# Kernel optimization log

Measured on AMD Instinct MI355X. Metric: run time of the kernel, lower is better.

## Reference

```python
import jax, jax.numpy as jnp
import numpy as np

N_TYPES = 4  # global / and / or / leaf node types (indep_weights)


def gcn_layer(x, W_stack, b, edge_src, edge_dst, edge_w, labels, num_nodes):
    # Per-node-type dense projection: compute all 4 projections, then select by label.
    # all4: [4, N, out]
    all4 = jnp.einsum('nd,kdo->kno', x, W_stack)
    support = jnp.take_along_axis(all4, labels[None, :, None].astype(jnp.int32), axis=0)[0]  # [N, out]
    # Sparse adjacency propagation: out[dst] += w * support[src]  (torch.spmm equivalent)
    msgs = support[edge_src] * edge_w[:, None]  # [E, out]
    agg = jax.ops.segment_sum(msgs, edge_dst, num_segments=num_nodes)
    return agg + b


def setup_inputs() -> dict:
    key = jax.random.key(0)
    ks = jax.random.split(key, 12)
    N, E = 50000, 1600000
    nfeat, nhid, nclass = 256, 256, 64
    x = jax.random.normal(ks[0], (N, nfeat), dtype=jnp.float32)
    edge_src = jax.random.randint(ks[1], (E,), 0, N, dtype=jnp.int32)
    edge_dst = jax.random.randint(ks[2], (E,), 0, N, dtype=jnp.int32)
    edge_w = jax.random.uniform(ks[3], (E,), dtype=jnp.float32)
    labels = jax.random.randint(ks[4], (N,), 0, N_TYPES, dtype=jnp.int32)
    def winit(k, fi, fo):
        s = 1.0 / np.sqrt(fo)
        return jax.random.uniform(k, (N_TYPES, fi, fo), minval=-s, maxval=s, dtype=jnp.float32)
    def binit(k, fo):
        s = 1.0 / np.sqrt(fo)
        return jax.random.uniform(k, (fo,), minval=-s, maxval=s, dtype=jnp.float32)
    return {
        'x': x, 'edge_src': edge_src, 'edge_dst': edge_dst, 'edge_w': edge_w, 'labels': labels,
        'W1': winit(ks[5], nfeat, nhid), 'b1': binit(ks[6], nhid),
        'W2': winit(ks[7], nhid, nhid), 'b2': binit(ks[8], nhid),
        'W3': winit(ks[9], nhid, nclass), 'b3': binit(ks[10], nclass),
    }


def reference(x, edge_src, edge_dst, edge_w, labels, W1, b1, W2, b2, W3, b3):
    N = x.shape[0]
    h = jax.nn.relu(gcn_layer(x, W1, b1, edge_src, edge_dst, edge_w, labels, N))
    # F.dropout with p=0 (module default) is identity
    h = jax.nn.relu(gcn_layer(h, W2, b2, edge_src, edge_dst, edge_w, labels, N))
    out = gcn_layer(h, W3, b3, edge_src, edge_dst, edge_w, labels, N)
    return out
```

## Files before the change

### kernel.cpp

```cpp
#include <hip/hip_runtime.h>
#include <hip/hip_bf16.h>

#define NT 4
#define FEAT 256
#define OUT3 64

typedef __bf16 bf16x8 __attribute__((ext_vector_type(8)));
typedef float  f32x4  __attribute__((ext_vector_type(4)));

__device__ inline unsigned int f2bf_bits(float f) {
    __hip_bfloat16 h = __float2bfloat16(f);
    unsigned short u;
    __builtin_memcpy(&u, &h, 2);
    return (unsigned int)u;
}
__device__ inline float bfl(unsigned int u) { return __uint_as_float(u << 16); }
__device__ inline float bfh(unsigned int u) { return __uint_as_float(u & 0xffff0000u); }
__device__ __host__ inline int nat_of(int p) {
    int lo = p & 63;
    return (p & ~63) | (((lo & 3) << 4) | (lo >> 2));
}

__global__ __launch_bounds__(512) void pass_a(const int* __restrict__ dst,
                                              const int* __restrict__ labels,
                                              int* __restrict__ bcnt, int* __restrict__ lc,
                                              int E, int N) {
    __shared__ int h[256];
    __shared__ int lh[NT];
    int tid = threadIdx.x;
    if (tid < 256) h[tid] = 0;
    if (tid < NT) lh[tid] = 0;
    __syncthreads();
    int base = blockIdx.x * 4096;
#pragma unroll
    for (int k = 0; k < 8; ++k) {
        int e = base + k * 512 + tid;
        if (e < E) atomicAdd(&h[((unsigned)dst[e]) >> 8], 1);
    }
#pragma unroll
    for (int k = 0; k < 8; ++k) {
        int i = base + k * 512 + tid;
        if (i < N) atomicAdd(&lh[labels[i]], 1);
    }
    __syncthreads();
    if (tid < 256) { int v = h[tid]; if (v) atomicAdd(&bcnt[tid], v); }
    if (tid < NT) { int v = lh[tid]; if (v) atomicAdd(&lc[tid], v); }
}

__global__ __launch_bounds__(256) void scan_master(
    const int* __restrict__ bcnt, const int* __restrict__ lc,
    int* __restrict__ boff, int* __restrict__ gcur, int* __restrict__ rowoff,
    int* __restrict__ lstart, int NB, int N, int E) {
    __shared__ int s[256];
    int tid = threadIdx.x;
    int own = (tid < NB) ? bcnt[tid] : 0;
    s[tid] = own;
    __syncthreads();
    for (int d = 1; d < 256; d <<= 1) {
        int v = (tid >= d) ? s[tid - d] : 0;
        __syncthreads();
        s[tid] += v;
        __syncthreads();
    }
    int excl = s[tid] - own;
    if (tid < NB) { boff[tid] = excl; gcur[tid] = excl; }
    if (tid == 0) {
        boff[NB] = E; rowoff[N] = E;
        int run = 0;
        for (int l = 0; l < NT; ++l) {
            lstart[l] = run;
            run += (lc[l] + 63) & ~63;
        }
    }
}

__global__ void scatter_nodes(const int* __restrict__ labels, const int* __restrict__ lstart,
                              int* __restrict__ lcur, int* __restrict__ iperm, int N) {
    int n = blockIdx.x * 256 + threadIdx.x;
    int lab = (n < N) ? labels[n] : -1;
    int lane = threadIdx.x & 63;
    for (int l = 0; l < NT; ++l) {
        unsigned long long m = __ballot(lab == l);
        if (m == 0ull) continue;
        int leader = __builtin_ctzll(m);
        int base = 0;
        if (lane == leader) base = atomicAdd(&lcur[l], (int)__popcll(m));
        base = __shfl(base, leader, 64);
        if (lab == l) {
            int prefix = (int)__popcll(m & ((1ull << lane) - 1ull));
            iperm[n] = lstart[l] + base + prefix;
        }
    }
}

__global__ __launch_bounds__(512) void fuse_a(
    const int* __restrict__ src, const int* __restrict__ dst, const float* __restrict__ w,
    const int* __restrict__ iperm, int* __restrict__ gcur, uint2* __restrict__ earr, int E,
    const float* __restrict__ x, unsigned short* __restrict__ actLo,
    unsigned short* __restrict__ actHi, int total4,
    const float* __restrict__ W1, const float* __restrict__ W2, const float* __restrict__ W3,
    const float* __restrict__ b1, const float* __restrict__ b2,
    unsigned short* __restrict__ W1b, unsigned short* __restrict__ W2b,
    unsigned short* __restrict__ W3b, float* __restrict__ biasPerm,
    int nbEB, int nbX) {
    int tid = threadIdx.x;
    int blk = (int)blockIdx.x;
    if (blk < nbEB) {
        __shared__ int h[256];
        __shared__ int basearr[256];
        if (tid < 256) h[tid] = 0;
        __syncthreads();
        int base = blk * 4096;
        int b[8], rank[8], px[8]; float wv[8];
#pragma unroll
        for (int k = 0; k < 8; ++k) {
            int e = base + k * 512 + tid;
            if (e < E) {
                int d = dst[e];
                b[k] = ((unsigned)d) >> 8;
                px[k] = iperm[src[e]] | ((d & 255) << 16);
                wv[k] = w[e];
                rank[k] = atomicAdd(&h[b[k]], 1);
            } else b[k] = -1;
        }
        __syncthreads();
        if (tid < 256) { int c = h[tid]; basearr[tid] = c ? atomicAdd(&gcur[tid], c) : 0; }
        __syncthreads();
#pragma unroll
        for (int k = 0; k < 8; ++k) {
            if (b[k] >= 0) {
                int pos = basearr[b[k]] + rank[k];
                earr[pos] = make_uint2((unsigned)px[k], __float_as_uint(wv[k]));
            }
        }
    } else if (blk < nbEB + nbX) {
        int i = (blk - nbEB) * 512 + tid;
        if (i < total4) {
            float4 v = ((const float4*)x)[i];
            unsigned int lo = f2bf_bits(v.x) | (f2bf_bits(v.y) << 16);
            unsigned int hi = f2bf_bits(v.z) | (f2bf_bits(v.w) << 16);
            int slot = iperm[i >> 6];
            unsigned short* dp = ((i & 63) >= 32) ? actHi : actLo;
            ((uint2*)dp)[(size_t)slot * 32 + (i & 31)] = make_uint2(lo, hi);
        }
    } else {
        const int S = NT * FEAT * FEAT;
        const int S3 = NT * FEAT * OUT3;
        int idx = (blk - nbEB - nbX) * 512 + tid;
        if (idx < 2 * S + S3) {
            const float* W; unsigned short* D; int OUTF; int t; bool remap;
            if (idx < S)          { W = W1; D = W1b; OUTF = FEAT; t = idx;         remap = false; }
            else if (idx < 2 * S) { W = W2; D = W2b; OUTF = FEAT; t = idx - S;     remap = true; }
            else                  { W = W3; D = W3b; OUTF = OUT3; t = idx - 2 * S; remap = true; }
            int n = t % OUTF;
            int r = t / OUTF;
            int j = r & 7, q = (r >> 3) & 3, k0 = (r >> 5) & 7, lab = r >> 8;
            int k_slot = k0 * 32 + q * 8 + j;
            int k_src = remap ? nat_of(k_slot) : k_slot;
            float f = W[((size_t)(lab * FEAT + k_src)) * OUTF + n];
            D[(((size_t)lab * 8 + k0) * OUTF + n) * 32 + q * 8 + j] = (unsigned short)f2bf_bits(f);
        } else {
            int p2 = idx - (2 * S + S3);
            if (p2 < 256) biasPerm[p2] = b1[nat_of(p2)];
            else if (p2 < 512) biasPerm[p2] = b2[nat_of(p2 - 256)];
        }
    }
}

__device__ void bucket_sort_body(int b, const uint2* __restrict__ earr,
                                 const int* __restrict__ boff, int* __restrict__ rowoff,
                                 unsigned int* __restrict__ edata, int N) {
    int s = boff[b], e = boff[b + 1];
    __shared__ int cnt[256], off[256];
    int tid = threadIdx.x;
    cnt[tid] = 0;
    __syncthreads();
    for (int i = s + tid; i < e; i += 256) atomicAdd(&cnt[(earr[i].x >> 16) & 255], 1);
    __syncthreads();
    off[tid] = cnt[tid];
    __syncthreads();
    for (int d = 1; d < 256; d <<= 1) {
        int v = (tid >= d) ? off[tid - d] : 0;
        __syncthreads();
        off[tid] += v;
        __syncthreads();
    }
    int excl = off[tid] - cnt[tid];
    int node = b * 256 + tid;
    if (node < N) rowoff[node] = s + excl;
    off[tid] = excl;
    __syncthreads();
    for (int i = s + tid; i < e; i += 256) {
        uint2 r = earr[i];
        int d = (r.x >> 16) & 255;
        int k = atomicAdd(&off[d], 1);
        edata[s + k] = (f2bf_bits(__uint_as_float(r.y)) << 16) | (r.x & 0xffff);
    }
}

__device__ void proj256_body(int gb,
                             const unsigned short* __restrict__ actLo,
                             const unsigned short* __restrict__ actHi,
                             const unsigned short* __restrict__ Wswz,
                             const int* __restrict__ lstart,
                             unsigned short* __restrict__ supLo,
                             unsigned short* __restrict__ supHi) {
    int warp = threadIdx.x >> 6;
    int lane = threadIdx.x & 63;
    int m0 = gb * 64;
    int lab = (m0 >= lstart[1]) + (m0 >= lstart[2]) + (m0 >= lstart[3]);
    int q = lane >> 4, c = lane & 15;
    int n0 = warp * 64;

    const unsigned short* aLo = actLo + (size_t)(m0 + c) * 128 + q * 8;
    const unsigned short* aHi = actHi + (size_t)(m0 + c) * 128 + q * 8;
    const unsigned short* bb = Wswz + (size_t)lab * FEAT * 256 + (size_t)(n0 + c) * 32 + q * 8;

    f32x4 acc[4][4] = {};
#pragma unroll
    for (int k0 = 0; k0 < 8; ++k0) {
        const unsigned short* abase = (k0 < 4) ? aLo : aHi;
        int koff = (k0 & 3) * 32;
        bf16x8 a[4];
#pragma unroll
        for (int t = 0; t < 4; ++t) a[t] = *(const bf16x8*)(abase + (size_t)t * 2048 + koff);
        const unsigned short* bk = bb + (size_t)k0 * 32 * 256;
#pragma unroll
        for (int u = 0; u < 4; ++u) {
            bf16x8 bfrag = *(const bf16x8*)(bk + u * 512);
#pragma unroll
            for (int t = 0; t < 4; ++t)
                acc[t][u] = __builtin_amdgcn_mfma_f32_16x16x32_bf16(a[t], bfrag, acc[t][u], 0, 0, 0);
        }
    }
    uint2* ov = (uint2*)((n0 >= 128) ? supHi : supLo);
    int cix = ((n0 & 64) >> 2) + c;
#pragma unroll
    for (int t = 0; t < 4; ++t) {
#pragma unroll
        for (int r = 0; r < 4; ++r) {
            int row = m0 + t * 16 + q * 4 + r;
            unsigned int lo = f2bf_bits(acc[t][0][r]) | (f2bf_bits(acc[t][1][r]) << 16);
            unsigned int hi = f2bf_bits(acc[t][2][r]) | (f2bf_bits(acc[t][3][r]) << 16);
            ov[(size_t)row * 32 + cix] = make_uint2(lo, hi);
        }
    }
}

__global__ __launch_bounds__(256) void fuse_b(
    const uint2* __restrict__ earr, const int* __restrict__ boff,
    int* __restrict__ rowoff, unsigned int* __restrict__ edata, int N, int NB,
    const unsigned short* __restrict__ actLo, const unsigned short* __restrict__ actHi,
    const unsigned short* __restrict__ Wswz, const int* __restrict__ lstart,
    unsigned short* __restrict__ supLo, unsigned short* __restrict__ supHi) {
    int blk = (int)blockIdx.x;
    if (blk < NB) bucket_sort_body(blk, earr, boff, rowoff, edata, N);
    else proj256_body(blk - NB, actLo, actHi, Wswz, lstart, supLo, supHi);
}

__global__ __launch_bounds__(256) void proj256_kernel(
    const unsigned short* __restrict__ actLo, const unsigned short* __restrict__ actHi,
    const unsigned short* __restrict__ Wswz, const int* __restrict__ lstart,
    unsigned short* __restrict__ supLo, unsigned short* __restrict__ supHi) {
    proj256_body((int)blockIdx.x, actLo, actHi, Wswz, lstart, supLo, supHi);
}

__global__ __launch_bounds__(256) void proj64_kernel(
    const unsigned short* __restrict__ actLo, const unsigned short* __restrict__ actHi,
    const unsigned short* __restrict__ Wswz, const int* __restrict__ lstart,
    unsigned short* __restrict__ outp) {
    int warp = threadIdx.x >> 6;
    int lane = threadIdx.x & 63;
    int m0 = blockIdx.x * 64;
    int lab = (m0 >= lstart[1]) + (m0 >= lstart[2]) + (m0 >= lstart[3]);
    int q = lane >> 4, c = lane & 15;
    int mb = m0 + warp * 16;

    const unsigned short* aLo = actLo + (size_t)(mb + c) * 128 + q * 8;
    const unsigned short* aHi = actHi + (size_t)(mb + c) * 128 + q * 8;
    const unsigned short* bb = Wswz + (size_t)lab * FEAT * OUT3 + (size_t)c * 32 + q * 8;

    f32x4 acc[4] = {};
#pragma unroll
    for (int k0 = 0; k0 < 8; ++k0) {
        const unsigned short* abase = (k0 < 4) ? aLo : aHi;
        bf16x8 a = *(const bf16x8*)(abase + (k0 & 3) * 32);
        const unsigned short* bk = bb + (size_t)k0 * 32 * OUT3;
#pragma unroll
        for (int u = 0; u < 4; ++u) {
            bf16x8 bfrag = *(const bf16x8*)(bk + u * 512);
            acc[u] = __builtin_amdgcn_mfma_f32_16x16x32_bf16(a, bfrag, acc[u], 0, 0, 0);
        }
    }
    uint2* ov = (uint2*)outp;
#pragma unroll
    for (int r = 0; r < 4; ++r) {
        int row = mb + q * 4 + r;
        unsigned int lo = f2bf_bits(acc[0][r]) | (f2bf_bits(acc[1][r]) << 16);
        unsigned int hi = f2bf_bits(acc[2][r]) | (f2bf_bits(acc[3][r]) << 16);
        ov[(size_t)row * 16 + c] = make_uint2(lo, hi);
    }
}

__global__ __launch_bounds__(256) void agg256h_kernel(
    const unsigned int* __restrict__ sup, const int* __restrict__ rowoff,
    const unsigned int* __restrict__ edata, const int* __restrict__ iperm,
    const float* __restrict__ biasHalf, unsigned int* __restrict__ outp, int N) {
    int warp = __builtin_amdgcn_readfirstlane((int)(threadIdx.x >> 6));
    int node = (int)blockIdx.x * 4 + warp;
    if (node >= N) return;
    int lane = threadIdx.x & 63;
    int s = __builtin_amdgcn_readfirstlane(rowoff[node]);
    int e = __builtin_amdgcn_readfirstlane(rowoff[node + 1]);
    int slot = __builtin_amdgcn_readfirstlane(iperm[node]);
    float a0 = 0.f, a1 = 0.f;
    int j = s;
    for (; j + 16 <= e; j += 16) {
        unsigned int ed[16], v[16];
#pragma unroll
        for (int u = 0; u < 16; ++u) ed[u] = edata[j + u];
#pragma unroll
        for (int u = 0; u < 16; ++u) v[u] = sup[(size_t)(ed[u] & 0xffff) * 64 + lane];
#pragma unroll
        for (int u = 0; u < 16; ++u) {
            float w = __uint_as_float(ed[u] & 0xffff0000u);
            a0 += w * bfl(v[u]); a1 += w * bfh(v[u]);
        }
    }
    if (j < e) {
        unsigned int ed[16], v[16]; float wm[16];
#pragma unroll
        for (int u = 0; u < 16; ++u) {
            int jj = j + u;
            int jc = (jj < e) ? jj : e - 1;
            ed[u] = edata[jc];
            wm[u] = (jj < e) ? __uint_as_float(ed[u] & 0xffff0000u) : 0.f;
        }
#pragma unroll
        for (int u = 0; u < 16; ++u) v[u] = sup[(size_t)(ed[u] & 0xffff) * 64 + lane];
#pragma unroll
        for (int u = 0; u < 16; ++u) { a0 += wm[u] * bfl(v[u]); a1 += wm[u] * bfh(v[u]); }
    }
    float2 b = ((const float2*)biasHalf)[lane];
    a0 = fmaxf(a0 + b.x, 0.f);
    a1 = fmaxf(a1 + b.y, 0.f);
    outp[(size_t)slot * 64 + lane] = f2bf_bits(a0) | (f2bf_bits(a1) << 16);
}

__global__ __launch_bounds__(256) void agg64_kernel(
    const unsigned short* __restrict__ sup, const int* __restrict__ rowoff,
    const unsigned int* __restrict__ edata, const float* __restrict__ b3,
    float* __restrict__ outp, int N) {
    int warp = __builtin_amdgcn_readfirstlane((int)(threadIdx.x >> 6));
    int node = (int)blockIdx.x * 4 + warp;
    if (node >= N) return;
    int lane = threadIdx.x & 63;
    int s = __builtin_amdgcn_readfirstlane(rowoff[node]);
    int e = __builtin_amdgcn_readfirstlane(rowoff[node + 1]);
    float a = 0.f;
    int j = s;
    for (; j + 8 <= e; j += 8) {
        unsigned int ed[8]; unsigned short v[8];
#pragma unroll
        for (int u = 0; u < 8; ++u) ed[u] = edata[j + u];
#pragma unroll
        for (int u = 0; u < 8; ++u) v[u] = sup[(size_t)(ed[u] & 0xffff) * 64 + lane];
#pragma unroll
        for (int u = 0; u < 8; ++u)
            a += __uint_as_float(ed[u] & 0xffff0000u) * __uint_as_float((unsigned int)v[u] << 16);
    }
    if (j < e) {
        unsigned int ed[8]; float wm[8]; unsigned short v[8];
#pragma unroll
        for (int u = 0; u < 8; ++u) {
            int jj = j + u;
            int jc = (jj < e) ? jj : e - 1;
            ed[u] = edata[jc];
            wm[u] = (jj < e) ? __uint_as_float(ed[u] & 0xffff0000u) : 0.f;
        }
#pragma unroll
        for (int u = 0; u < 8; ++u) v[u] = sup[(size_t)(ed[u] & 0xffff) * 64 + lane];
#pragma unroll
        for (int u = 0; u < 8; ++u)
            a += wm[u] * __uint_as_float((unsigned int)v[u] << 16);
    }
    int natp = (((lane & 3) << 4) | (lane >> 2));
    outp[(size_t)node * 64 + natp] = a + b3[natp];
}

extern "C" void kernel_launch(void* const* d_in, const int* in_sizes, int n_in,
                              void* d_out, int out_size, void* d_ws, size_t ws_size,
                              hipStream_t stream) {
    const float* x        = (const float*)d_in[0];
    const int*   edge_src = (const int*)d_in[1];
    const int*   edge_dst = (const int*)d_in[2];
    const float* edge_w   = (const float*)d_in[3];
    const int*   labels   = (const int*)d_in[4];
    const float* W1 = (const float*)d_in[5];
    const float* b1 = (const float*)d_in[6];
    const float* W2 = (const float*)d_in[7];
    const float* b2 = (const float*)d_in[8];
    const float* W3 = (const float*)d_in[9];
    const float* b3 = (const float*)d_in[10];

    const int N = in_sizes[0] / FEAT;
    const int E = in_sizes[1];
    const int NB = (N + 255) >> 8;
    const int G64 = (N + NT * 64 + 63) / 64;
    const int slotCap = G64 * 64;

    char* p = (char*)d_ws;
    auto alloc = [&](size_t bytes) -> char* {
        char* r = p;
        p += (bytes + 255) & ~(size_t)255;
        return r;
    };
    unsigned short* bufA = (unsigned short*)alloc((size_t)slotCap * FEAT * 2);
    unsigned short* bufB = (unsigned short*)alloc((size_t)slotCap * FEAT * 2);
    unsigned short* W1b  = (unsigned short*)alloc((size_t)NT * FEAT * FEAT * 2);
    unsigned short* W2b  = (unsigned short*)alloc((size_t)NT * FEAT * FEAT * 2);
    unsigned short* W3b  = (unsigned short*)alloc((size_t)NT * FEAT * OUT3 * 2);
    float*        biasPerm = (float*)alloc(512 * 4);
    int*          rowoff = (int*)alloc((size_t)(N + 1) * 4);
    unsigned int* edata  = (unsigned int*)alloc((size_t)E * 4);
    int*          iperm  = (int*)alloc((size_t)N * 4);
    int*          counters = (int*)alloc(264 * 4);
    int*          boff   = (int*)alloc(257 * 4);
    int*          gcur   = (int*)alloc(256 * 4);
    int*          lstart = (int*)alloc(64);
    int* bcnt = counters;
    int* lc   = counters + 256;
    int* lcur = counters + 260;

    unsigned short* actLo = bufA;
    unsigned short* actHi = bufA + (size_t)slotCap * 128;
    unsigned short* supLo = bufB;
    unsigned short* supHi = bufB + (size_t)slotCap * 128;
    uint2* earr = (uint2*)d_out;

    const int nbEB = (E + 4095) / 4096;
    const int total4 = N * 64;
    const int nbX = (total4 + 511) / 512;
    const int totW = 2 * NT * FEAT * FEAT + NT * FEAT * OUT3 + 512;
    const int nbW = (totW + 511) / 512;

    hipMemsetAsync(counters, 0, 264 * 4, stream);
    pass_a<<<nbEB, 512, 0, stream>>>(edge_dst, labels, bcnt, lc, E, N);
    scan_master<<<1, 256, 0, stream>>>(bcnt, lc, boff, gcur, rowoff, lstart, NB, N, E);
    scatter_nodes<<<(N + 255) / 256, 256, 0, stream>>>(labels, lstart, lcur, iperm, N);
    fuse_a<<<nbEB + nbX + nbW, 512, 0, stream>>>(
        edge_src, edge_dst, edge_w, iperm, gcur, earr, E,
        x, actLo, actHi, total4,
        W1, W2, W3, b1, b2, W1b, W2b, W3b, biasPerm, nbEB, nbX);

    const int aggGrid = (N + 3) / 4;
    fuse_b<<<NB + G64, 256, 0, stream>>>(earr, boff, rowoff, edata, N, NB,
                                         actLo, actHi, W1b, lstart, supLo, supHi);
    agg256h_kernel<<<aggGrid, 256, 0, stream>>>((const unsigned int*)supLo, rowoff, edata, iperm,
                                                biasPerm + 0, (unsigned int*)actLo, N);
    agg256h_kernel<<<aggGrid, 256, 0, stream>>>((const unsigned int*)supHi, rowoff, edata, iperm,
                                                biasPerm + 128, (unsigned int*)actHi, N);
    proj256_kernel<<<G64, 256, 0, stream>>>(actLo, actHi, W2b, lstart, supLo, supHi);
    agg256h_kernel<<<aggGrid, 256, 0, stream>>>((const unsigned int*)supLo, rowoff, edata, iperm,
                                                biasPerm + 256, (unsigned int*)actLo, N);
    agg256h_kernel<<<aggGrid, 256, 0, stream>>>((const unsigned int*)supHi, rowoff, edata, iperm,
                                                biasPerm + 384, (unsigned int*)actHi, N);
    proj64_kernel<<<G64, 256, 0, stream>>>(actLo, actHi, W3b, lstart, bufB);
    agg64_kernel<<<aggGrid, 256, 0, stream>>>(bufB, rowoff, edata, b3, (float*)d_out, N);
}
```

Before: 482.3 us.

## Use fixed-capacity dst buckets to drop histogram pass; add nontemporal loads/stores

```diff
diff --git a/kernel.cpp b/kernel.cpp
--- a/kernel.cpp
+++ b/kernel.cpp
@@ -4,9 +4,11 @@
 #define NT 4
 #define FEAT 256
 #define OUT3 64
+#define CAP 10240
 
 typedef __bf16 bf16x8 __attribute__((ext_vector_type(8)));
 typedef float  f32x4  __attribute__((ext_vector_type(4)));
+typedef unsigned long long u64;
 
 __device__ inline unsigned int f2bf_bits(float f) {
     __hip_bfloat16 h = __float2bfloat16(f);
@@ -20,62 +22,38 @@
     int lo = p & 63;
     return (p & ~63) | (((lo & 3) << 4) | (lo >> 2));
 }
-
-__global__ __launch_bounds__(512) void pass_a(const int* __restrict__ dst,
-                                              const int* __restrict__ labels,
-                                              int* __restrict__ bcnt, int* __restrict__ lc,
-                                              int E, int N) {
-    __shared__ int h[256];
+__device__ inline u64 ntl64(const void* p) { return __builtin_nontemporal_load((const u64*)p); }
+__device__ inline int ntl32i(const void* p) { return __builtin_nontemporal_load((const int*)p); }
+__device__ inline float ntlf(const void* p) { return __builtin_nontemporal_load((const float*)p); }
+__device__ inline void nts64(void* p, u64 v) { __builtin_nontemporal_store(v, (u64*)p); }
+__device__ inline void nts32(void* p, unsigned int v) { __builtin_nontemporal_store(v, (unsigned int*)p); }
+__device__ inline void ntsf(void* p, float v) { __builtin_nontemporal_store(v, (float*)p); }
+__device__ inline void nts16(void* p, unsigned short v) { __builtin_nontemporal_store(v, (unsigned short*)p); }
+
+__global__ __launch_bounds__(512) void label_hist(const int* __restrict__ labels,
+                                                  int* __restrict__ lc, int N) {
     __shared__ int lh[NT];
     int tid = threadIdx.x;
-    if (tid < 256) h[tid] = 0;
     if (tid < NT) lh[tid] = 0;
     __syncthreads();
     int base = blockIdx.x * 4096;
-#pragma unroll
-    for (int k = 0; k < 8; ++k) {
-        int e = base + k * 512 + tid;
-        if (e < E) atomicAdd(&h[((unsigned)dst[e]) >> 8], 1);
-    }
 #pragma unroll
     for (int k = 0; k < 8; ++k) {
         int i = base + k * 512 + tid;
         if (i < N) atomicAdd(&lh[labels[i]], 1);
     }
     __syncthreads();
-    if (tid < 256) { int v = h[tid]; if (v) atomicAdd(&bcnt[tid], v); }
     if (tid < NT) { int v = lh[tid]; if (v) atomicAdd(&lc[tid], v); }
 }
 
-__global__ __launch_bounds__(256) void scan_master(
-    const int* __restrict__ bcnt, const int* __restrict__ lc,
-    int* __restrict__ boff, int* __restrict__ gcur, int* __restrict__ rowoff,
-    int* __restrict__ lstart, int NB, int N, int E) {
-    __shared__ int s[256];
-    int tid = threadIdx.x;
-    int own = (tid < NB) ? bcnt[tid] : 0;
-    s[tid] = own;
-    __syncthreads();
-    for (int d = 1; d < 256; d <<= 1) {
-        int v = (tid >= d) ? s[tid - d] : 0;
-        __syncthreads();
-        s[tid] += v;
-        __syncthreads();
-    }
-    int excl = s[tid] - own;
-    if (tid < NB) { boff[tid] = excl; gcur[tid] = excl; }
-    if (tid == 0) {
-        boff[NB] = E; rowoff[N] = E;
+__global__ void scatter_nodes(const int* __restrict__ labels, const int* __restrict__ lc,
+                              int* __restrict__ lcur, int* __restrict__ iperm, int N) {
+    int lst[NT];
+    {
         int run = 0;
-        for (int l = 0; l < NT; ++l) {
-            lstart[l] = run;
-            run += (lc[l] + 63) & ~63;
-        }
-    }
-}
-
-__global__ void scatter_nodes(const int* __restrict__ labels, const int* __restrict__ lstart,
-                              int* __restrict__ lcur, int* __restrict__ iperm, int N) {
+#pragma unroll
+        for (int l = 0; l < NT; ++l) { lst[l] = run; run += (lc[l] + 63) & ~63; }
+    }
     int n = blockIdx.x * 256 + threadIdx.x;
     int lab = (n < N) ? labels[n] : -1;
     int lane = threadIdx.x & 63;
@@ -88,14 +66,14 @@
         base = __shfl(base, leader, 64);
         if (lab == l) {
             int prefix = (int)__popcll(m & ((1ull << lane) - 1ull));
-            iperm[n] = lstart[l] + base + prefix;
+            iperm[n] = lst[l] + base + prefix;
         }
     }
 }
 
 __global__ __launch_bounds__(512) void fuse_a(
     const int* __restrict__ src, const int* __restrict__ dst, const float* __restrict__ w,
-    const int* __restrict__ iperm, int* __restrict__ gcur, uint2* __restrict__ earr, int E,
+    const int* __restrict__ iperm, int* __restrict__ gcur, u64* __restrict__ earr, int E,
     const float* __restrict__ x, unsigned short* __restrict__ actLo,
     unsigned short* __restrict__ actHi, int total4,
     const float* __restrict__ W1, const float* __restrict__ W2, const float* __restrict__ W3,
@@ -116,10 +94,10 @@
         for (int k = 0; k < 8; ++k) {
             int e = base + k * 512 + tid;
             if (e < E) {
-                int d = dst[e];
+                int d = ntl32i(dst + e);
                 b[k] = ((unsigned)d) >> 8;
-                px[k] = iperm[src[e]] | ((d & 255) << 16);
-                wv[k] = w[e];
+                px[k] = iperm[ntl32i(src + e)] | ((d & 255) << 16);
+                wv[k] = ntlf(w + e);
                 rank[k] = atomicAdd(&h[b[k]], 1);
             } else b[k] = -1;
         }
@@ -129,19 +107,22 @@
 #pragma unroll
         for (int k = 0; k < 8; ++k) {
             if (b[k] >= 0) {
-                int pos = basearr[b[k]] + rank[k];
-                earr[pos] = make_uint2((unsigned)px[k], __float_as_uint(wv[k]));
+                size_t pos = (size_t)b[k] * CAP + basearr[b[k]] + rank[k];
+                nts64(&earr[pos], (u64)(unsigned)px[k] | ((u64)__float_as_uint(wv[k]) << 32));
             }
         }
     } else if (blk < nbEB + nbX) {
         int i = (blk - nbEB) * 512 + tid;
         if (i < total4) {
-            float4 v = ((const float4*)x)[i];
-            unsigned int lo = f2bf_bits(v.x) | (f2bf_bits(v.y) << 16);
-            unsigned int hi = f2bf_bits(v.z) | (f2bf_bits(v.w) << 16);
+            const u64* xp = (const u64*)x + (size_t)i * 2;
+            u64 w0 = ntl64(xp), w1 = ntl64(xp + 1);
+            float f0 = __uint_as_float((unsigned)w0), f1 = __uint_as_float((unsigned)(w0 >> 32));
+            float f2 = __uint_as_float((unsigned)w1), f3 = __uint_as_float((unsigned)(w1 >> 32));
+            unsigned int lo = f2bf_bits(f0) | (f2bf_bits(f1) << 16);
+            unsigned int hi = f2bf_bits(f2) | (f2bf_bits(f3) << 16);
             int slot = iperm[i >> 6];
-            unsigned short* dp = ((i & 63) >= 32) ? actHi : actLo;
-            ((uint2*)dp)[(size_t)slot * 32 + (i & 31)] = make_uint2(lo, hi);
+            u64* dp = (u64*)(((i & 63) >= 32) ? actHi : actLo);
+            nts64(dp + (size_t)slot * 32 + (i & 31), (u64)lo | ((u64)hi << 32));
         }
     } else {
         const int S = NT * FEAT * FEAT;
@@ -157,8 +138,9 @@
             int j = r & 7, q = (r >> 3) & 3, k0 = (r >> 5) & 7, lab = r >> 8;
             int k_slot = k0 * 32 + q * 8 + j;
             int k_src = remap ? nat_of(k_slot) : k_slot;
-            float f = W[((size_t)(lab * FEAT + k_src)) * OUTF + n];
-            D[(((size_t)lab * 8 + k0) * OUTF + n) * 32 + q * 8 + j] = (unsigned short)f2bf_bits(f);
+            float f = ntlf(&W[((size_t)(lab * FEAT + k_src)) * OUTF + n]);
+            nts16(&D[(((size_t)lab * 8 + k0) * OUTF + n) * 32 + q * 8 + j],
+                  (unsigned short)f2bf_bits(f));
         } else {
             int p2 = idx - (2 * S + S3);
             if (p2 < 256) biasPerm[p2] = b1[nat_of(p2)];
@@ -167,17 +149,23 @@
     }
 }
 
-__device__ void bucket_sort_body(int b, const uint2* __restrict__ earr,
-                                 const int* __restrict__ boff, int* __restrict__ rowoff,
+__device__ void bucket_sort_body(int b, const u64* __restrict__ earr,
+                                 const int* __restrict__ gcur,
+                                 int* __restrict__ rs, int* __restrict__ re,
                                  unsigned int* __restrict__ edata, int N) {
-    int s = boff[b], e = boff[b + 1];
-    __shared__ int cnt[256], off[256];
+    int s = b * CAP;
+    int cnt = gcur[b];
+    int e = s + cnt;
+    __shared__ int cntS[256], off[256];
     int tid = threadIdx.x;
-    cnt[tid] = 0;
-    __syncthreads();
-    for (int i = s + tid; i < e; i += 256) atomicAdd(&cnt[(earr[i].x >> 16) & 255], 1);
-    __syncthreads();
-    off[tid] = cnt[tid];
+    cntS[tid] = 0;
+    __syncthreads();
+    for (int i = s + tid; i < e; i += 256) {
+        u64 r = ntl64(&earr[i]);
+        atomicAdd(&cntS[((unsigned)r >> 16) & 255], 1);
+    }
+    __syncthreads();
+    off[tid] = cntS[tid];
     __syncthreads();
     for (int d = 1; d < 256; d <<= 1) {
         int v = (tid >= d) ? off[tid - d] : 0;
@@ -185,16 +173,18 @@
         off[tid] += v;
         __syncthreads();
     }
-    int excl = off[tid] - cnt[tid];
+    int excl = off[tid] - cntS[tid];
     int node = b * 256 + tid;
-    if (node < N) rowoff[node] = s + excl;
+    if (node < N) { rs[node] = s + excl; re[node] = s + excl + cntS[tid]; }
     off[tid] = excl;
     __syncthreads();
     for (int i = s + tid; i < e; i += 256) {
-        uint2 r = earr[i];
-        int d = (r.x >> 16) & 255;
-        int k = atomicAdd(&off[d], 1);
-        edata[s + k] = (f2bf_bits(__uint_as_float(r.y)) << 16) | (r.x & 0xffff);
+        u64 r = ntl64(&earr[i]);
+        unsigned int lo32 = (unsigned int)r;
+        int d2 = (lo32 >> 16) & 255;
+        int k = atomicAdd(&off[d2], 1);
+        nts32(&edata[s + k],
+              (f2bf_bits(__uint_as_float((unsigned)(r >> 32))) << 16) | (lo32 & 0xffff));
     }
 }
 
@@ -202,13 +192,14 @@
                              const unsigned short* __restrict__ actLo,
                              const unsigned short* __restrict__ actHi,
                              const unsigned short* __restrict__ Wswz,
-                             const int* __restrict__ lstart,
+                             const int* __restrict__ lc,
                              unsigned short* __restrict__ supLo,
                              unsigned short* __restrict__ supHi) {
     int warp = threadIdx.x >> 6;
     int lane = threadIdx.x & 63;
     int m0 = gb * 64;
-    int lab = (m0 >= lstart[1]) + (m0 >= lstart[2]) + (m0 >= lstart[3]);
+    int c0 = (lc[0] + 63) & ~63, c1 = (lc[1] + 63) & ~63, c2 = (lc[2] + 63) & ~63;
+    int lab = (m0 >= c0) + (m0 >= c0 + c1) + (m0 >= c0 + c1 + c2);
     int q = lane >> 4, c = lane & 15;
     int n0 = warp * 64;
 
@@ -233,7 +224,7 @@
                 acc[t][u] = __builtin_amdgcn_mfma_f32_16x16x32_bf16(a[t], bfrag, acc[t][u], 0, 0, 0);
         }
     }
-    uint2* ov = (uint2*)((n0 >= 128) ? supHi : supLo);
+    u64* ov = (u64*)((n0 >= 128) ? supHi : supLo);
     int cix = ((n0 & 64) >> 2) + c;
 #pragma unroll
     for (int t = 0; t < 4; ++t) {
@@ -242,37 +233,39 @@
             int row = m0 + t * 16 + q * 4 + r;
             unsigned int lo = f2bf_bits(acc[t][0][r]) | (f2bf_bits(acc[t][1][r]) << 16);
             unsigned int hi = f2bf_bits(acc[t][2][r]) | (f2bf_bits(acc[t][3][r]) << 16);
-            ov[(size_t)row * 32 + cix] = make_uint2(lo, hi);
+            nts64(&ov[(size_t)row * 32 + cix], (u64)lo | ((u64)hi << 32));
         }
     }
 }
 
 __global__ __launch_bounds__(256) void fuse_b(
-    const uint2* __restrict__ earr, const int* __restrict__ boff,
-    int* __restrict__ rowoff, unsigned int* __restrict__ edata, int N, int NB,
+    const u64* __restrict__ earr, const int* __restrict__ gcur,
+    int* __restrict__ rs, int* __restrict__ re, unsigned int* __restrict__ edata,
+    int N, int NB,
     const unsigned short* __restrict__ actLo, const unsigned short* __restrict__ actHi,
-    const unsigned short* __restrict__ Wswz, const int* __restrict__ lstart,
+    const unsigned short* __restrict__ Wswz, const int* __restrict__ lc,
     unsigned short* __restrict__ supLo, unsigned short* __restrict__ supHi) {
     int blk = (int)blockIdx.x;
-    if (blk < NB) bucket_sort_body(blk, earr, boff, rowoff, edata, N);
-    else proj256_body(blk - NB, actLo, actHi, Wswz, lstart, supLo, supHi);
+    if (blk < NB) bucket_sort_body(blk, earr, gcur, rs, re, edata, N);
+    else proj256_body(blk - NB, actLo, actHi, Wswz, lc, supLo, supHi);
 }
 
 __global__ __launch_bounds__(256) void proj256_kernel(
     const unsigned short* __restrict__ actLo, const unsigned short* __restrict__ actHi,
-    const unsigned short* __restrict__ Wswz, const int* __restrict__ lstart,
+    const unsigned short* __restrict__ Wswz, const int* __restrict__ lc,
     unsigned short* __restrict__ supLo, unsigned short* __restrict__ supHi) {
-    proj256_body((int)blockIdx.x, actLo, actHi, Wswz, lstart, supLo, supHi);
+    proj256_body((int)blockIdx.x, actLo, actHi, Wswz, lc, supLo, supHi);
 }
 
 __global__ __launch_bounds__(256) void proj64_kernel(
     const unsigned short* __restrict__ actLo, const unsigned short* __restrict__ actHi,
-    const unsigned short* __restrict__ Wswz, const int* __restrict__ lstart,
+    const unsigned short* __restrict__ Wswz, const int* __restrict__ lc,
     unsigned short* __restrict__ outp) {
     int warp = threadIdx.x >> 6;
     int lane = threadIdx.x & 63;
     int m0 = blockIdx.x * 64;
-    int lab = (m0 >= lstart[1]) + (m0 >= lstart[2]) + (m0 >= lstart[3]);
+    int c0 = (lc[0] + 63) & ~63, c1 = (lc[1] + 63) & ~63, c2 = (lc[2] + 63) & ~63;
+    int lab = (m0 >= c0) + (m0 >= c0 + c1) + (m0 >= c0 + c1 + c2);
     int q = lane >> 4, c = lane & 15;
     int mb = m0 + warp * 16;
 
@@ -292,26 +285,27 @@
             acc[u] = __builtin_amdgcn_mfma_f32_16x16x32_bf16(a, bfrag, acc[u], 0, 0, 0);
         }
     }
-    uint2* ov = (uint2*)outp;
+    u64* ov = (u64*)outp;
 #pragma unroll
     for (int r = 0; r < 4; ++r) {
         int row = mb + q * 4 + r;
         unsigned int lo = f2bf_bits(acc[0][r]) | (f2bf_bits(acc[1][r]) << 16);
         unsigned int hi = f2bf_bits(acc[2][r]) | (f2bf_bits(acc[3][r]) << 16);
-        ov[(size_t)row * 16 + c] = make_uint2(lo, hi);
+        nts64(&ov[(size_t)row * 16 + c], (u64)lo | ((u64)hi << 32));
     }
 }
 
 __global__ __launch_bounds__(256) void agg256h_kernel(
-    const unsigned int* __restrict__ sup, const int* __restrict__ rowoff,
-    const unsigned int* __restrict__ edata, const int* __restrict__ iperm,
-    const float* __restrict__ biasHalf, unsigned int* __restrict__ outp, int N) {
+    const unsigned int* __restrict__ sup, const int* __restrict__ rs,
+    const int* __restrict__ re, const unsigned int* __restrict__ edata,
+    const int* __restrict__ iperm, const float* __restrict__ biasHalf,
+    unsigned int* __restrict__ outp, int N) {
     int warp = __builtin_amdgcn_readfirstlane((int)(threadIdx.x >> 6));
     int node = (int)blockIdx.x * 4 + warp;
     if (node >= N) return;
     int lane = threadIdx.x & 63;
-    int s = __builtin_amdgcn_readfirstlane(rowoff[node]);
-    int e = __builtin_amdgcn_readfirstlane(rowoff[node + 1]);
+    int s = __builtin_amdgcn_readfirstlane(rs[node]);
+    int e = __builtin_amdgcn_readfirstlane(re[node]);
     int slot = __builtin_amdgcn_readfirstlane(iperm[node]);
     float a0 = 0.f, a1 = 0.f;
     int j = s;
@@ -344,19 +338,19 @@
     float2 b = ((const float2*)biasHalf)[lane];
     a0 = fmaxf(a0 + b.x, 0.f);
     a1 = fmaxf(a1 + b.y, 0.f);
-    outp[(size_t)slot * 64 + lane] = f2bf_bits(a0) | (f2bf_bits(a1) << 16);
+    nts32(&outp[(size_t)slot * 64 + lane], f2bf_bits(a0) | (f2bf_bits(a1) << 16));
 }
 
 __global__ __launch_bounds__(256) void agg64_kernel(
-    const unsigned short* __restrict__ sup, const int* __restrict__ rowoff,
-    const unsigned int* __restrict__ edata, const float* __restrict__ b3,
-    float* __restrict__ outp, int N) {
+    const unsigned short* __restrict__ sup, const int* __restrict__ rs,
+    const int* __restrict__ re, const unsigned int* __restrict__ edata,
+    const float* __restrict__ b3, float* __restrict__ outp, int N) {
     int warp = __builtin_amdgcn_readfirstlane((int)(threadIdx.x >> 6));
     int node = (int)blockIdx.x * 4 + warp;
     if (node >= N) return;
     int lane = threadIdx.x & 63;
-    int s = __builtin_amdgcn_readfirstlane(rowoff[node]);
-    int e = __builtin_amdgcn_readfirstlane(rowoff[node + 1]);
+    int s = __builtin_amdgcn_readfirstlane(rs[node]);
+    int e = __builtin_amdgcn_readfirstlane(re[node]);
     float a = 0.f;
     int j = s;
     for (; j + 8 <= e; j += 8) {
@@ -385,7 +379,7 @@
             a += wm[u] * __uint_as_float((unsigned int)v[u] << 16);
     }
     int natp = (((lane & 3) << 4) | (lane >> 2));
-    outp[(size_t)node * 64 + natp] = a + b3[natp];
+    ntsf(&outp[(size_t)node * 64 + natp], a + b3[natp]);
 }
 
 extern "C" void kernel_launch(void* const* d_in, const int* in_sizes, int n_in,
@@ -421,14 +415,13 @@
     unsigned short* W2b  = (unsigned short*)alloc((size_t)NT * FEAT * FEAT * 2);
     unsigned short* W3b  = (unsigned short*)alloc((size_t)NT * FEAT * OUT3 * 2);
     float*        biasPerm = (float*)alloc(512 * 4);
-    int*          rowoff = (int*)alloc((size_t)(N + 1) * 4);
-    unsigned int* edata  = (unsigned int*)alloc((size_t)E * 4);
+    int*          rs     = (int*)alloc((size_t)N * 4);
+    int*          re     = (int*)alloc((size_t)N * 4);
+    unsigned int* edata  = (unsigned int*)alloc((size_t)NB * CAP * 4);
+    u64*          earr   = (u64*)alloc((size_t)NB * CAP * 8);
     int*          iperm  = (int*)alloc((size_t)N * 4);
     int*          counters = (int*)alloc(264 * 4);
-    int*          boff   = (int*)alloc(257 * 4);
-    int*          gcur   = (int*)alloc(256 * 4);
-    int*          lstart = (int*)alloc(64);
-    int* bcnt = counters;
+    int* gcur = counters;
     int* lc   = counters + 256;
     int* lcur = counters + 260;
 
@@ -436,7 +429,6 @@
     unsigned short* actHi = bufA + (size_t)slotCap * 128;
     unsigned short* supLo = bufB;
     unsigned short* supHi = bufB + (size_t)slotCap * 128;
-    uint2* earr = (uint2*)d_out;
 
     const int nbEB = (E + 4095) / 4096;
     const int total4 = N * 64;
@@ -445,26 +437,25 @@
     const int nbW = (totW + 511) / 512;
 
     hipMemsetAsync(counters, 0, 264 * 4, stream);
-    pass_a<<<nbEB, 512, 0, stream>>>(edge_dst, labels, bcnt, lc, E, N);
-    scan_master<<<1, 256, 0, stream>>>(bcnt, lc, boff, gcur, rowoff, lstart, NB, N, E);
-    scatter_nodes<<<(N + 255) / 256, 256, 0, stream>>>(labels, lstart, lcur, iperm, N);
+    label_hist<<<(N + 4095) / 4096, 512, 0, stream>>>(labels, lc, N);
+    scatter_nodes<<<(N + 255) / 256, 256, 0, stream>>>(labels, lc, lcur, iperm, N);
     fuse_a<<<nbEB + nbX + nbW, 512, 0, stream>>>(
         edge_src, edge_dst, edge_w, iperm, gcur, earr, E,
         x, actLo, actHi, total4,
         W1, W2, W3, b1, b2, W1b, W2b, W3b, biasPerm, nbEB, nbX);
 
     const int aggGrid = (N + 3) / 4;
-    fuse_b<<<NB + G64, 256, 0, stream>>>(earr, boff, rowoff, edata, N, NB,
-                                         actLo, actHi, W1b, lstart, supLo, supHi);
-    agg256h_kernel<<<aggGrid, 256, 0, stream>>>((const unsigned int*)supLo, rowoff, edata, iperm,
+    fuse_b<<<NB + G64, 256, 0, stream>>>(earr, gcur, rs, re, edata, N, NB,
+                                         actLo, actHi, W1b, lc, supLo, supHi);
+    agg256h_kernel<<<aggGrid, 256, 0, stream>>>((const unsigned int*)supLo, rs, re, edata, iperm,
                                                 biasPerm + 0, (unsigned int*)actLo, N);
-    agg256h_kernel<<<aggGrid, 256, 0, stream>>>((const unsigned int*)supHi, rowoff, edata, iperm,
+    agg256h_kernel<<<aggGrid, 256, 0, stream>>>((const unsigned int*)supHi, rs, re, edata, iperm,
                                                 biasPerm + 128, (unsigned int*)actHi, N);
-    proj256_kernel<<<G64, 256, 0, stream>>>(actLo, actHi, W2b, lstart, supLo, supHi);
-    agg256h_kernel<<<aggGrid, 256, 0, stream>>>((const unsigned int*)supLo, rowoff, edata, iperm,
+    proj256_kernel<<<G64, 256, 0, stream>>>(actLo, actHi, W2b, lc, supLo, supHi);
+    agg256h_kernel<<<aggGrid, 256, 0, stream>>>((const unsigned int*)supLo, rs, re, edata, iperm,
                                                 biasPerm + 256, (unsigned int*)actLo, N);
-    agg256h_kernel<<<aggGrid, 256, 0, stream>>>((const unsigned int*)supHi, rowoff, edata, iperm,
+    agg256h_kernel<<<aggGrid, 256, 0, stream>>>((const unsigned int*)supHi, rs, re, edata, iperm,
                                                 biasPerm + 384, (unsigned int*)actHi, N);
-    proj64_kernel<<<G64, 256, 0, stream>>>(actLo, actHi, W3b, lstart, bufB);
-    agg64_kernel<<<aggGrid, 256, 0, stream>>>(bufB, rowoff, edata, b3, (float*)d_out, N);
-}
+    proj64_kernel<<<G64, 256, 0, stream>>>(actLo, actHi, W3b, lc, bufB);
+    agg64_kernel<<<aggGrid, 256, 0, stream>>>(bufB, rs, re, edata, b3, (float*)d_out, N);
+}
```

Result: slower. 560.0 us (+16.1%).
